# Optimization experiments

Measured on AMD Instinct MI355X. Metric: run time of the kernel, lower is better.

## Reference

```python
import jax, jax.numpy as jnp
import numpy as np

B, V, CIN, H, W = 2, 4, 256, 96, 96
COUT, VS = 32, 64


def setup_inputs() -> dict:
    key = jax.random.key(0)
    k1, k2, k3, k4, k5 = jax.random.split(key, 5)
    features = jax.random.normal(k1, (B, V, CIN, H, W), dtype=jnp.float32)
    proj_matricies = jax.random.normal(k2, (B, V, 3, 4), dtype=jnp.float32)
    coord_volumes = jax.random.normal(k3, (B, VS, VS, VS, 3), dtype=jnp.float32) * 1000.0
    W_proc = jax.random.normal(k4, (COUT, CIN), dtype=jnp.float32) * 0.05
    b_proc = jax.random.normal(k5, (COUT,), dtype=jnp.float32) * 0.01
    return {"features": features, "proj_matricies": proj_matricies,
            "coord_volumes": coord_volumes, "W_proc": W_proc, "b_proc": b_proc}


def _bilinear_sample(feat, x, y):
    # feat: [C, H, W]; x, y: [N] pixel coords (align_corners=True mapping already applied)
    Hh, Ww = feat.shape[1], feat.shape[2]
    x0 = jnp.floor(x).astype(jnp.int32); x1 = x0 + 1
    y0 = jnp.floor(y).astype(jnp.int32); y1 = y0 + 1
    wx1 = x - x0; wx0 = 1.0 - wx1
    wy1 = y - y0; wy0 = 1.0 - wy1

    def gather(xi, yi):
        valid = ((xi >= 0) & (xi < Ww) & (yi >= 0) & (yi < Hh)).astype(feat.dtype)
        xc = jnp.clip(xi, 0, Ww - 1); yc = jnp.clip(yi, 0, Hh - 1)
        return feat[:, yc, xc] * valid  # [C, N] (zeros padding)

    return (gather(x0, y0) * (wx0 * wy0)
            + gather(x1, y0) * (wx1 * wy0)
            + gather(x0, y1) * (wx0 * wy1)
            + gather(x1, y1) * (wx1 * wy1))


def reference(features, proj_matricies, coord_volumes, W_proc, b_proc):
    b, v, cin, h, w = features.shape
    vs = coord_volumes.shape[1]
    # 1x1 conv (process_feature)
    feats = jnp.einsum('bvchw,oc->bvohw', features, W_proc) + b_proc[None, None, :, None, None]
    c = feats.shape[2]
    # homogeneous 3D grid points: [B, N, 4]
    pts = coord_volumes.reshape(b, -1, 3)
    pts_h = jnp.concatenate([pts, jnp.ones(pts.shape[:-1] + (1,), pts.dtype)], axis=-1)
    # project to image plane: [B, V, N, 3] homogeneous (u, v, w)
    proj_pts = jnp.einsum('bvij,bnj->bvni', proj_matricies, pts_h)
    wz = proj_pts[..., 2]
    invalid = wz <= 0.0
    wz_safe = jnp.where(wz == 0.0, 1.0, wz)
    u = proj_pts[..., 0] / wz_safe
    ve = proj_pts[..., 1] / wz_safe
    # normalized grid coords (faithful to original: x divided by feature_shape[0]=H, y by feature_shape[1]=W)
    gx = 2.0 * (u / h - 0.5)
    gy = 2.0 * (ve / w - 0.5)
    # align_corners=True pixel coords: x indexes width, y indexes height
    px = (gx + 1.0) * 0.5 * (w - 1)
    py = (gy + 1.0) * 0.5 * (h - 1)
    # sample per (batch, view): [B, V, C, N]
    sampled = jax.vmap(jax.vmap(_bilinear_sample))(feats, px, py)
    sampled = jnp.where(invalid[:, :, None, :], 0.0, sampled)
    # softmax over views per (b, c, voxel), weighted sum
    weights = jax.nn.softmax(sampled, axis=1)
    vol = jnp.sum(sampled * weights, axis=1)  # [B, C, N]
    return vol.reshape(b, c, vs, vs, vs)
```

## Files before the change

kernel.cpp:

```cpp
#include <hip/hip_runtime.h>
#include <hip/hip_bf16.h>

#define CIN   256
#define COUT  32
#define IMG_H 96
#define IMG_W 96
#define HW    (IMG_H*IMG_W)
#define NB    2
#define NV    4
#define VSZ   64
#define NVOX  (VSZ*VSZ*VSZ)

__global__ __launch_bounds__(256) void conv1x1_kernel(
    const float* __restrict__ features,
    const float* __restrict__ Wp,
    const float* __restrict__ bp,
    __hip_bfloat16* __restrict__ out)
{
    __shared__ float Wt[CIN*COUT];
    const int tid = threadIdx.x;
    #pragma unroll
    for (int i = 0; i < CIN*COUT/256; ++i) {
        int idx = i*256 + tid;
        int c = idx >> 5, o = idx & 31;
        Wt[idx] = Wp[o*CIN + c];
    }
    __syncthreads();

    const int og   = tid >> 6;
    const int lane = tid & 63;
    const int bv   = blockIdx.y;
    const int px   = blockIdx.x*64 + lane;
    const float* f = features + (size_t)bv*CIN*HW + px;

    float acc[8];
    #pragma unroll
    for (int j = 0; j < 8; ++j) acc[j] = bp[og*8 + j];

    #pragma unroll 8
    for (int c = 0; c < CIN; ++c) {
        const float x = f[(size_t)c*HW];
        const float4 w0 = *(const float4*)(&Wt[c*COUT + og*8]);
        const float4 w1 = *(const float4*)(&Wt[c*COUT + og*8 + 4]);
        acc[0] += x*w0.x; acc[1] += x*w0.y; acc[2] += x*w0.z; acc[3] += x*w0.w;
        acc[4] += x*w1.x; acc[5] += x*w1.y; acc[6] += x*w1.z; acc[7] += x*w1.w;
    }

    union { uint4 u4; __hip_bfloat16 h[8]; } pk;
    #pragma unroll
    for (int j = 0; j < 8; ++j) pk.h[j] = __float2bfloat16(acc[j]);
    *(uint4*)(out + ((size_t)(bv*HW + px))*COUT + og*8) = pk.u4;
}

__global__ __launch_bounds__(256) void volgen_kernel(
    const __hip_bfloat16* __restrict__ feats,
    const float* __restrict__ proj,
    const float* __restrict__ coords,
    float* __restrict__ out)
{
    __shared__ float T[COUT*65];
    const int tid = threadIdx.x;
    const int vl  = tid >> 2;
    const int cg  = tid & 3;
    const int b   = blockIdx.y;
    const int n   = blockIdx.x*64 + vl;

    const float* cp = coords + ((size_t)b*NVOX + n)*3;
    const float X = cp[0], Y = cp[1], Z = cp[2];

    float A[8], Bs[8];
    #pragma unroll
    for (int j = 0; j < 8; ++j) { A[j] = 0.f; Bs[j] = 0.f; }

    #pragma unroll
    for (int v = 0; v < NV; ++v) {
        const float* P = proj + (size_t)(b*NV + v)*12;
        const float wz = P[8]*X + P[9]*Y + P[10]*Z + P[11];
        float s[8];
        #pragma unroll
        for (int j = 0; j < 8; ++j) s[j] = 0.f;
        bool did = false;

        if (wz > 0.f) {
            const float rz = __builtin_amdgcn_rcpf(wz);
            const float px = (P[0]*X + P[1]*Y + P[2]*Z + P[3]) * rz * (95.f/96.f);
            const float py = (P[4]*X + P[5]*Y + P[6]*Z + P[7]) * rz * (95.f/96.f);
            const float fx0 = floorf(px), fy0 = floorf(py);
            const int x0 = (int)fx0, y0 = (int)fy0, x1 = x0+1, y1 = y0+1;
            const bool vx0 = (x0 >= 0) & (x0 < IMG_W);
            const bool vx1 = (x1 >= 0) & (x1 < IMG_W);
            const bool vy0 = (y0 >= 0) & (y0 < IMG_H);
            const bool vy1 = (y1 >= 0) & (y1 < IMG_H);
            if ((vx0 | vx1) & (vy0 | vy1)) {
                did = true;
                const float wx1 = px - fx0, wx0 = 1.f - wx1;
                const float wy1 = py - fy0, wy0 = 1.f - wy1;
                const __hip_bfloat16* base =
                    feats + ((size_t)(b*NV + v)*HW)*COUT + cg*8;
                #pragma unroll
                for (int corner = 0; corner < 4; ++corner) {
                    const int cx = (corner & 1) ? x1 : x0;
                    const int cy = (corner & 2) ? y1 : y0;
                    const bool ok = ((corner & 1) ? vx1 : vx0) &
                                    ((corner & 2) ? vy1 : vy0);
                    if (ok) {
                        const float w = ((corner & 1) ? wx1 : wx0) *
                                        ((corner & 2) ? wy1 : wy0);
                        const uint4 t = *(const uint4*)(base + (size_t)(cy*IMG_W + cx)*COUT);
                        const unsigned tu[4] = { t.x, t.y, t.z, t.w };
                        #pragma unroll
                        for (int k = 0; k < 4; ++k) {
                            s[2*k]   += w * __uint_as_float(tu[k] << 16);
                            s[2*k+1] += w * __uint_as_float(tu[k] & 0xffff0000u);
                        }
                    }
                }
            }
        }

        if (did) {
            #pragma unroll
            for (int j = 0; j < 8; ++j) {
                const float e = __expf(s[j]);
                A[j] += e; Bs[j] += s[j]*e;
            }
        } else {
            #pragma unroll
            for (int j = 0; j < 8; ++j) A[j] += 1.f;
        }
    }

    #pragma unroll
    for (int j = 0; j < 8; ++j)
        T[(cg*8 + j)*65 + vl] = Bs[j] * __builtin_amdgcn_rcpf(A[j]);
    __syncthreads();

    const size_t ob = (size_t)b*COUT*NVOX + (size_t)blockIdx.x*64;
    #pragma unroll
    for (int i = 0; i < 8; ++i) {
        const int idx = i*256 + tid;
        const int ch = idx >> 6, vx = idx & 63;
        out[ob + (size_t)ch*NVOX + vx] = T[ch*65 + vx];
    }
}

extern "C" void kernel_launch(void* const* d_in, const int* in_sizes, int n_in,
                              void* d_out, int out_size, void* d_ws, size_t ws_size,
                              hipStream_t stream)
{
    const float* features = (const float*)d_in[0];
    const float* proj     = (const float*)d_in[1];
    const float* coords   = (const float*)d_in[2];
    const float* Wp       = (const float*)d_in[3];
    const float* bp       = (const float*)d_in[4];
    float* out = (float*)d_out;
    __hip_bfloat16* featsT = (__hip_bfloat16*)d_ws;

    hipLaunchKernelGGL(conv1x1_kernel, dim3(HW/64, NB*NV), dim3(256), 0, stream,
                       features, Wp, bp, featsT);
    hipLaunchKernelGGL(volgen_kernel, dim3(NVOX/64, NB), dim3(256), 0, stream,
                       featsT, proj, coords, out);
}
```

Before: 211.2 us.

## Split conv input channels across waves and batch all bilinear gathers branch-free

The 1x1 conv now has each wave handle a quarter of the input channels for all 32 outputs, so every feature element is loaded once per block instead of once per output group. Partial sums are then reduced through shared memory. The volume kernel computes all 16 corner offsets and weights up front, with clamped indices and zero weights for invalid corners, then issues every gather before the softmax math. This removes divergent branches and gives more loads in flight, at the cost of more registers and always-executed loads and exps.

```diff
diff --git a/kernel.cpp b/kernel.cpp
--- a/kernel.cpp
+++ b/kernel.cpp
@@ -18,38 +18,70 @@
     __hip_bfloat16* __restrict__ out)
 {
     __shared__ float Wt[CIN*COUT];
+    __shared__ float Pp[4*64*36];
     const int tid = threadIdx.x;
     #pragma unroll
     for (int i = 0; i < CIN*COUT/256; ++i) {
         int idx = i*256 + tid;
-        int c = idx >> 5, o = idx & 31;
-        Wt[idx] = Wp[o*CIN + c];
+        Wt[idx] = Wp[(idx & 31)*CIN + (idx >> 5)];
     }
     __syncthreads();
 
-    const int og   = tid >> 6;
+    const int w    = tid >> 6;
     const int lane = tid & 63;
     const int bv   = blockIdx.y;
-    const int px   = blockIdx.x*64 + lane;
-    const float* f = features + (size_t)bv*CIN*HW + px;
+    const int px0  = blockIdx.x*64;
+    const float* f = features + (size_t)bv*CIN*HW + (size_t)(w*64)*HW + px0 + lane;
 
-    float acc[8];
+    float acc[32];
     #pragma unroll
-    for (int j = 0; j < 8; ++j) acc[j] = bp[og*8 + j];
+    for (int o = 0; o < 32; ++o) acc[o] = (w == 0) ? bp[o] : 0.f;
 
-    #pragma unroll 8
-    for (int c = 0; c < CIN; ++c) {
-        const float x = f[(size_t)c*HW];
-        const float4 w0 = *(const float4*)(&Wt[c*COUT + og*8]);
-        const float4 w1 = *(const float4*)(&Wt[c*COUT + og*8 + 4]);
-        acc[0] += x*w0.x; acc[1] += x*w0.y; acc[2] += x*w0.z; acc[3] += x*w0.w;
-        acc[4] += x*w1.x; acc[5] += x*w1.y; acc[6] += x*w1.z; acc[7] += x*w1.w;
+    const float* wrow = &Wt[(w*64)*COUT];
+    for (int cc = 0; cc < 64; cc += 16) {
+        float x[16];
+        #pragma unroll
+        for (int i = 0; i < 16; ++i)
+            x[i] = f[(size_t)(cc + i)*HW];
+        #pragma unroll
+        for (int i = 0; i < 16; ++i) {
+            const float4* wr = (const float4*)(wrow + (size_t)(cc + i)*COUT);
+            const float4 w0 = wr[0], w1 = wr[1], w2 = wr[2], w3 = wr[3];
+            const float xi = x[i];
+            acc[ 0] += xi*w0.x; acc[ 1] += xi*w0.y; acc[ 2] += xi*w0.z; acc[ 3] += xi*w0.w;
+            acc[ 4] += xi*w1.x; acc[ 5] += xi*w1.y; acc[ 6] += xi*w1.z; acc[ 7] += xi*w1.w;
+            acc[ 8] += xi*w2.x; acc[ 9] += xi*w2.y; acc[10] += xi*w2.z; acc[11] += xi*w2.w;
+            acc[12] += xi*w3.x; acc[13] += xi*w3.y; acc[14] += xi*w3.z; acc[15] += xi*w3.w;
+            const float4* wr2 = wr + 4;
+            const float4 w4 = wr2[0], w5 = wr2[1], w6 = wr2[2], w7 = wr2[3];
+            acc[16] += xi*w4.x; acc[17] += xi*w4.y; acc[18] += xi*w4.z; acc[19] += xi*w4.w;
+            acc[20] += xi*w5.x; acc[21] += xi*w5.y; acc[22] += xi*w5.z; acc[23] += xi*w5.w;
+            acc[24] += xi*w6.x; acc[25] += xi*w6.y; acc[26] += xi*w6.z; acc[27] += xi*w6.w;
+            acc[28] += xi*w7.x; acc[29] += xi*w7.y; acc[30] += xi*w7.z; acc[31] += xi*w7.w;
+        }
     }
 
+    #pragma unroll
+    for (int j = 0; j < 8; ++j)
+        *(float4*)(&Pp[(w*64 + lane)*36 + j*4]) =
+            make_float4(acc[4*j], acc[4*j+1], acc[4*j+2], acc[4*j+3]);
+    __syncthreads();
+
+    const int px = tid >> 2, cg = tid & 3;
+    float r[8];
+    #pragma unroll
+    for (int j = 0; j < 8; ++j) r[j] = 0.f;
+    #pragma unroll
+    for (int ww = 0; ww < 4; ++ww) {
+        const float4* p = (const float4*)(&Pp[(ww*64 + px)*36 + cg*8]);
+        const float4 a = p[0], b2 = p[1];
+        r[0] += a.x;  r[1] += a.y;  r[2] += a.z;  r[3] += a.w;
+        r[4] += b2.x; r[5] += b2.y; r[6] += b2.z; r[7] += b2.w;
+    }
     union { uint4 u4; __hip_bfloat16 h[8]; } pk;
     #pragma unroll
-    for (int j = 0; j < 8; ++j) pk.h[j] = __float2bfloat16(acc[j]);
-    *(uint4*)(out + ((size_t)(bv*HW + px))*COUT + og*8) = pk.u4;
+    for (int j = 0; j < 8; ++j) pk.h[j] = __float2bfloat16(r[j]);
+    *(uint4*)(out + ((size_t)(bv*HW + px0 + px))*COUT + cg*8) = pk.u4;
 }
 
 __global__ __launch_bounds__(256) void volgen_kernel(
@@ -68,65 +100,66 @@
     const float* cp = coords + ((size_t)b*NVOX + n)*3;
     const float X = cp[0], Y = cp[1], Z = cp[2];
 
+    int   off[NV][4];
+    float wgt[NV][4];
+    #pragma unroll
+    for (int v = 0; v < NV; ++v) {
+        const float* P = proj + (size_t)(b*NV + v)*12;
+        const float wz = P[8]*X + P[9]*Y + P[10]*Z + P[11];
+        const bool  vz = wz > 0.f;
+        const float rz = __builtin_amdgcn_rcpf(wz);
+        float px = (P[0]*X + P[1]*Y + P[2]*Z + P[3]) * rz * (95.f/96.f);
+        float py = (P[4]*X + P[5]*Y + P[6]*Z + P[7]) * rz * (95.f/96.f);
+        px = vz ? px : 0.f;  py = vz ? py : 0.f;
+        px = fminf(fmaxf(px, -1.0e6f), 1.0e6f);
+        py = fminf(fmaxf(py, -1.0e6f), 1.0e6f);
+        const float fx0 = floorf(px), fy0 = floorf(py);
+        const int x0 = (int)fx0, y0 = (int)fy0, x1 = x0+1, y1 = y0+1;
+        const float wx1 = px - fx0, wx0 = 1.f - wx1;
+        const float wy1 = py - fy0, wy0 = 1.f - wy1;
+        const bool vx0 = (unsigned)x0 < (unsigned)IMG_W;
+        const bool vx1 = (unsigned)x1 < (unsigned)IMG_W;
+        const bool vy0 = (unsigned)y0 < (unsigned)IMG_H;
+        const bool vy1 = (unsigned)y1 < (unsigned)IMG_H;
+        const int cx0 = min(max(x0, 0), IMG_W-1), cx1 = min(max(x1, 0), IMG_W-1);
+        const int cy0 = min(max(y0, 0), IMG_H-1), cy1 = min(max(y1, 0), IMG_H-1);
+        const int base = ((b*NV + v)*HW)*COUT + cg*8;
+        off[v][0] = base + (cy0*IMG_W + cx0)*COUT;  wgt[v][0] = (vz & vx0 & vy0) ? wx0*wy0 : 0.f;
+        off[v][1] = base + (cy0*IMG_W + cx1)*COUT;  wgt[v][1] = (vz & vx1 & vy0) ? wx1*wy0 : 0.f;
+        off[v][2] = base + (cy1*IMG_W + cx0)*COUT;  wgt[v][2] = (vz & vx0 & vy1) ? wx0*wy1 : 0.f;
+        off[v][3] = base + (cy1*IMG_W + cx1)*COUT;  wgt[v][3] = (vz & vx1 & vy1) ? wx1*wy1 : 0.f;
+    }
+
+    uint4 t[NV][4];
+    #pragma unroll
+    for (int v = 0; v < NV; ++v)
+        #pragma unroll
+        for (int c = 0; c < 4; ++c)
+            t[v][c] = *(const uint4*)(feats + off[v][c]);
+
     float A[8], Bs[8];
     #pragma unroll
     for (int j = 0; j < 8; ++j) { A[j] = 0.f; Bs[j] = 0.f; }
 
     #pragma unroll
     for (int v = 0; v < NV; ++v) {
-        const float* P = proj + (size_t)(b*NV + v)*12;
-        const float wz = P[8]*X + P[9]*Y + P[10]*Z + P[11];
         float s[8];
         #pragma unroll
         for (int j = 0; j < 8; ++j) s[j] = 0.f;
-        bool did = false;
-
-        if (wz > 0.f) {
-            const float rz = __builtin_amdgcn_rcpf(wz);
-            const float px = (P[0]*X + P[1]*Y + P[2]*Z + P[3]) * rz * (95.f/96.f);
-            const float py = (P[4]*X + P[5]*Y + P[6]*Z + P[7]) * rz * (95.f/96.f);
-            const float fx0 = floorf(px), fy0 = floorf(py);
-            const int x0 = (int)fx0, y0 = (int)fy0, x1 = x0+1, y1 = y0+1;
-            const bool vx0 = (x0 >= 0) & (x0 < IMG_W);
-            const bool vx1 = (x1 >= 0) & (x1 < IMG_W);
-            const bool vy0 = (y0 >= 0) & (y0 < IMG_H);
-            const bool vy1 = (y1 >= 0) & (y1 < IMG_H);
-            if ((vx0 | vx1) & (vy0 | vy1)) {
-                did = true;
-                const float wx1 = px - fx0, wx0 = 1.f - wx1;
-                const float wy1 = py - fy0, wy0 = 1.f - wy1;
-                const __hip_bfloat16* base =
-                    feats + ((size_t)(b*NV + v)*HW)*COUT + cg*8;
-                #pragma unroll
-                for (int corner = 0; corner < 4; ++corner) {
-                    const int cx = (corner & 1) ? x1 : x0;
-                    const int cy = (corner & 2) ? y1 : y0;
-                    const bool ok = ((corner & 1) ? vx1 : vx0) &
-                                    ((corner & 2) ? vy1 : vy0);
-                    if (ok) {
-                        const float w = ((corner & 1) ? wx1 : wx0) *
-                                        ((corner & 2) ? wy1 : wy0);
-                        const uint4 t = *(const uint4*)(base + (size_t)(cy*IMG_W + cx)*COUT);
-                        const unsigned tu[4] = { t.x, t.y, t.z, t.w };
-                        #pragma unroll
-                        for (int k = 0; k < 4; ++k) {
-                            s[2*k]   += w * __uint_as_float(tu[k] << 16);
-                            s[2*k+1] += w * __uint_as_float(tu[k] & 0xffff0000u);
-                        }
-                    }
-                }
+        #pragma unroll
+        for (int c = 0; c < 4; ++c) {
+            const float w = wgt[v][c];
+            const unsigned tu[4] = { t[v][c].x, t[v][c].y, t[v][c].z, t[v][c].w };
+            #pragma unroll
+            for (int k = 0; k < 4; ++k) {
+                s[2*k]   += w * __uint_as_float(tu[k] << 16);
+                s[2*k+1] += w * __uint_as_float(tu[k] & 0xffff0000u);
             }
         }
-
-        if (did) {
-            #pragma unroll
-            for (int j = 0; j < 8; ++j) {
-                const float e = __expf(s[j]);
-                A[j] += e; Bs[j] += s[j]*e;
-            }
-        } else {
-            #pragma unroll
-            for (int j = 0; j < 8; ++j) A[j] += 1.f;
+        #pragma unroll
+        for (int j = 0; j < 8; ++j) {
+            const float e = __expf(s[j]);
+            A[j] += e;  Bs[j] += s[j]*e;
         }
     }
 
```

Result: slower. 222.0 us (+5.1%).
